# Kernel tuning notes

Measured on AMD Instinct MI355X. Metric: run time of the kernel, lower is better.

The kernel has to match this reference:

```python
import jax, jax.numpy as jnp
import numpy as np

B, S, D, H = 2, 2048, 1024, 16
HD = D // H  # 64


def setup_inputs() -> dict:
    key = jax.random.key(0)
    ks = jax.random.split(key, 12)
    scale = 1.0 / np.sqrt(D)
    inp = {
        "input_query": jax.random.normal(ks[0], (B, S, D), jnp.float32),
        "input_key": jax.random.normal(ks[1], (B, S, D), jnp.float32),
        "input_value": jax.random.normal(ks[2], (B, S, D), jnp.float32),
        "mask": jax.random.randint(ks[3], (B, 1, S), 0, 2, jnp.int32),
        # torch nn.Linear params: y = x @ W.T + b, W shape (out, in)
        "wq": jax.random.uniform(ks[4], (D, D), jnp.float32, -scale, scale),
        "bq": jax.random.uniform(ks[5], (D,), jnp.float32, -scale, scale),
        "wk": jax.random.uniform(ks[6], (D, D), jnp.float32, -scale, scale),
        "bk": jax.random.uniform(ks[7], (D,), jnp.float32, -scale, scale),
        "wv": jax.random.uniform(ks[8], (D, D), jnp.float32, -scale, scale),
        "bv": jax.random.uniform(ks[9], (D,), jnp.float32, -scale, scale),
        "wo": jax.random.uniform(ks[10], (D, D), jnp.float32, -scale, scale),
        "bo": jax.random.uniform(ks[11], (D,), jnp.float32, -scale, scale),
    }
    return inp


def _split_heads(x):
    # (B, S, D) -> (B, H, S, HD)
    return x.reshape(B, S, H, HD).transpose(0, 2, 1, 3)


def reference(input_query, input_key, input_value, mask, wq, bq, wk, bk, wv, bv, wo, bo):
    q = _split_heads(input_query @ wq.T + bq)
    k = _split_heads(input_key @ wk.T + bk)
    v = _split_heads(input_value @ wv.T + bv)

    # scaled dot-product attention (materializes [B,H,S,S] as the original does)
    scores = jnp.einsum("bhqd,bhkd->bhqk", q, k) / np.sqrt(HD).astype(np.float32)
    # mask: (B, 1, S) -> unsqueeze(1) -> (B, 1, 1, S); fill -1e9 where mask == 0
    m = mask[:, None, :, :]
    scores = jnp.where(m == 0, jnp.float32(-1e9), scores)
    p_attn = jax.nn.softmax(scores, axis=-1)  # dropout is identity (rate 0 / eval)

    out = jnp.einsum("bhqk,bhkd->bhqd", p_attn, v)
    out = out.transpose(0, 2, 1, 3).reshape(B, S, D)
    return out @ wo.T + bo
```

## Files before the change

kernel.cpp:

```cpp
#include <hip/hip_runtime.h>
#include <math.h>

#define BB 2
#define SS 2048
#define DD 1024
#define HH 16
#define HD 64

typedef short short8 __attribute__((ext_vector_type(8)));
typedef float floatx4 __attribute__((ext_vector_type(4)));
typedef float floatx16 __attribute__((ext_vector_type(16)));
typedef unsigned int uintx2 __attribute__((ext_vector_type(2)));

__device__ inline ushort f2bf_rne(float x) {
    union { float f; unsigned u; } v; v.f = x;
    unsigned r = v.u + 0x7FFFu + ((v.u >> 16) & 1u);
    return (ushort)(r >> 16);
}
__device__ inline unsigned cvt_pk_bf16(float lo, float hi) {
    unsigned r;
    asm("v_cvt_pk_bf16_f32 %0, %1, %2" : "=v"(r) : "v"(lo), "v"(hi));
    return r;
}
__device__ inline short8 mk_pf(uintx2 x, uintx2 y) {
    union { unsigned u[4]; short8 s; } t;
    t.u[0] = x[0]; t.u[1] = y[0]; t.u[2] = x[1]; t.u[3] = y[1];
    return t.s;
}

#define GLD16(gp, lp) __builtin_amdgcn_global_load_lds( \
    (const __attribute__((address_space(1))) void*)(gp), \
    (__attribute__((address_space(3))) void*)(lp), 16, 0, 0)

__global__ __launch_bounds__(256)
void convert_bf16(const float* __restrict__ xq, const float* __restrict__ xk,
                  const float* __restrict__ xv,
                  const float* __restrict__ wq, const float* __restrict__ wk,
                  const float* __restrict__ wv, const float* __restrict__ wo,
                  ushort* __restrict__ Xq, ushort* __restrict__ Xk,
                  ushort* __restrict__ Xv,
                  ushort* __restrict__ Wq, ushort* __restrict__ Wk,
                  ushort* __restrict__ Wv, ushort* __restrict__ Wo)
{
    const int z = blockIdx.z;
    const size_t i = ((size_t)blockIdx.x * 256 + threadIdx.x) * 8;

    const float* src;
    ushort* dst;
    size_t off;
    if (z < 3) {
        src = (z == 0) ? xq : (z == 1) ? xk : xv;
        dst = (z == 0) ? Xq : (z == 1) ? Xk : Xv;
        off = i;
    } else {
        const int seg = (int)(i >> 20);
        off = i & ((1u << 20) - 1);
        src = (seg == 0) ? wq : (seg == 1) ? wk : (seg == 2) ? wv : wo;
        dst = (seg == 0) ? Wq : (seg == 1) ? Wk : (seg == 2) ? Wv : Wo;
    }
    float x[8];
    *(float4*)&x[0] = *(const float4*)(src + off);
    *(float4*)&x[4] = *(const float4*)(src + off + 4);
    short8 h8;
#pragma unroll
    for (int j = 0; j < 8; ++j) h8[j] = (short)f2bf_rne(x[j]);
    *(short8*)&dst[off] = h8;
}

__global__ __launch_bounds__(256, 3)
void qkv_gemm(const ushort* __restrict__ Xq, const ushort* __restrict__ Xk,
              const ushort* __restrict__ Xv,
              const ushort* __restrict__ Wq, const ushort* __restrict__ Wk,
              const ushort* __restrict__ Wv,
              const float* __restrict__ bq, const float* __restrict__ bk,
              const float* __restrict__ bv, const int* __restrict__ mask,
              ushort* __restrict__ Qo, ushort* __restrict__ Ko,
              ushort* __restrict__ Vo, float qscale)
{
    __shared__ __align__(16) ushort SMEM[8704];
#define ALDS(r, c) SMEM[(r) * 32 + (c)]
#define BLDS(r, c) SMEM[4096 + (r) * 32 + (c)]
#define EPI(r, c)  SMEM[(r) * 136 + (c)]

    const int z   = blockIdx.z;
    const int tid = threadIdx.x;

    const ushort* X    = (z == 0) ? Xq : (z == 1) ? Xk : Xv;
    const ushort* W    = (z == 0) ? Wq : (z == 1) ? Wk : Wv;
    const float*  bias = (z == 0) ? bq : (z == 1) ? bk : bv;
    const float   osc  = (z == 0) ? qscale : 1.0f;

    const int lane = tid & 63;
    const int wave = tid >> 6;
    const int wr = wave >> 1;
    const int wc = wave & 1;
    const int lt = lane & 15;
    const int lq = lane >> 4;
    const int m0 = blockIdx.y * 128;
    const int n0 = blockIdx.x * 128;

    floatx4 acc[4][4];
#pragma unroll
    for (int mi = 0; mi < 4; ++mi)
#pragma unroll
        for (int ni = 0; ni < 4; ++ni) acc[mi][ni] = (floatx4)0.0f;

    const int srow = tid >> 2;
    const int sc   = (tid & 3) << 3;
    const ushort* gA0 = X + (size_t)(m0 + srow) * DD + sc;
    const ushort* gA1 = X + (size_t)(m0 + 64 + srow) * DD + sc;
    const ushort* gB0 = W + (size_t)(n0 + srow) * DD + sc;
    const ushort* gB1 = W + (size_t)(n0 + 64 + srow) * DD + sc;

    for (int k0 = 0; k0 < DD; k0 += 32) {
        __syncthreads();
        GLD16(gA0 + k0, &ALDS(srow, sc));
        GLD16(gA1 + k0, &ALDS(64 + srow, sc));
        GLD16(gB0 + k0, &BLDS(srow, sc));
        GLD16(gB1 + k0, &BLDS(64 + srow, sc));
        __syncthreads();

        short8 af[4], bf_[4];
#pragma unroll
        for (int mi = 0; mi < 4; ++mi)
            af[mi] = *(const short8*)&ALDS(wr * 64 + mi * 16 + lt, lq * 8);
#pragma unroll
        for (int ni = 0; ni < 4; ++ni)
            bf_[ni] = *(const short8*)&BLDS(wc * 64 + ni * 16 + lt, lq * 8);

#pragma unroll
        for (int mi = 0; mi < 4; ++mi)
#pragma unroll
            for (int ni = 0; ni < 4; ++ni)
                acc[mi][ni] = __builtin_amdgcn_mfma_f32_16x16x32_bf16(af[mi], bf_[ni], acc[mi][ni], 0, 0, 0);
    }

    float bbv[4];
#pragma unroll
    for (int ni = 0; ni < 4; ++ni) bbv[ni] = bias[n0 + wc * 64 + ni * 16 + lt];

    if (z == 2) {
#pragma unroll
        for (int half = 0; half < 2; ++half) {
            __syncthreads();
            if (wc == half) {
#pragma unroll
                for (int mi = 0; mi < 4; ++mi) {
                    const int mb  = m0 + wr * 64 + mi * 16 + lq * 4;
                    const int bb_ = mb >> 11;
                    const int s   = mb & (SS - 1);
                    const int4 mm = *(const int4*)(mask + bb_ * SS + s);
                    const float mf[4] = {(float)mm.x, (float)mm.y, (float)mm.z, (float)mm.w};
#pragma unroll
                    for (int ni = 0; ni < 4; ++ni)
#pragma unroll
                        for (int r = 0; r < 4; ++r)
                            EPI(ni * 16 + lt, wr * 64 + mi * 16 + lq * 4 + r) =
                                f2bf_rne((acc[mi][ni][r] + bbv[ni]) * mf[r]);
                }
            }
            __syncthreads();
            const int b_ = m0 >> 11;
            const int sB = m0 & (SS - 1);
#pragma unroll
            for (int u = 0; u < 4; ++u) {
                const int idx = u * 256 + tid;
                const int row = idx >> 4;
                const int sg  = (idx & 15) << 3;
                const short8 v = *(const short8*)&EPI(row, sg);
                const int n = n0 + half * 64 + row;
                const int h = n >> 6;
                *(short8*)&Vo[((size_t)(b_ * HH + h) * HD + (n & 63)) * SS + sB + sg] = v;
            }
        }
    } else {
        ushort* C = z ? Ko : Qo;
#pragma unroll
        for (int half = 0; half < 2; ++half) {
            __syncthreads();
            if (wr == half) {
#pragma unroll
                for (int mi = 0; mi < 4; ++mi) {
                    const int mb  = m0 + half * 64 + mi * 16 + lq * 4;
                    const int bb_ = mb >> 11;
                    const int s   = mb & (SS - 1);
                    float mf[4] = {1.0f, 1.0f, 1.0f, 1.0f};
                    if (z == 1) {
                        const int4 mm = *(const int4*)(mask + bb_ * SS + s);
                        mf[0] = (float)mm.x; mf[1] = (float)mm.y;
                        mf[2] = (float)mm.z; mf[3] = (float)mm.w;
                    }
#pragma unroll
                    for (int ni = 0; ni < 4; ++ni)
#pragma unroll
                        for (int r = 0; r < 4; ++r)
                            EPI(mi * 16 + lq * 4 + r, wc * 64 + ni * 16 + lt) =
                                f2bf_rne((acc[mi][ni][r] + bbv[ni]) * osc * mf[r]);
                }
            }
            __syncthreads();
#pragma unroll
            for (int u = 0; u < 4; ++u) {
                const int idx = u * 256 + tid;
                const int row = idx >> 4;
                const int cg  = (idx & 15) << 3;
                const short8 v = *(const short8*)&EPI(row, cg);
                const int m = m0 + half * 64 + row;
                const int n = n0 + cg;
                const int h = n >> 6;
                const int b_ = m >> 11;
                const int s  = m & (SS - 1);
                *(short8*)&C[((size_t)(b_ * HH + h) * SS + s) * HD + (n & 63)] = v;
            }
        }
    }
#undef ALDS
#undef BLDS
#undef EPI
}

#define LDV 68

__global__ __launch_bounds__(256, 4)
void attn_mfma(const ushort* __restrict__ Qb, const ushort* __restrict__ Kb,
               const ushort* __restrict__ Vt, const int* __restrict__ mask,
               ushort* __restrict__ Ob)
{
    __shared__ __align__(16) ushort KVlds[4][64][LDV];
    __shared__ int Wsum[4];

    const int tid  = threadIdx.x;
    const int lane = tid & 63;
    const int wave = tid >> 6;
    const int ll   = lane & 31;
    const int hi   = lane >> 5;
    const int qh   = wave & 1;
    const int ks   = wave >> 1;

    const int bid    = blockIdx.x;
    const int xcd    = bid & 7;
    const int slot   = bid >> 3;
    const int bhloc  = slot >> 5;
    const int qi     = slot & 31;
    const int bh     = xcd * 4 + bhloc;
    const int b      = bh >> 4;
    const int q0     = qi * 64;

    const size_t sbase = (size_t)bh * SS * HD;
    const size_t vbase = (size_t)bh * HD * SS;

    {
        const int4 ma = *(const int4*)(mask + b * SS + tid * 8);
        const int4 mb = *(const int4*)(mask + b * SS + tid * 8 + 4);
        int s = ma.x + ma.y + ma.z + ma.w + mb.x + mb.y + mb.z + mb.w;
#pragma unroll
        for (int w = 32; w >= 1; w >>= 1) s += __shfl_xor(s, w);
        if (lane == 0) Wsum[wave] = s;
    }

    short8 ones;
#pragma unroll
    for (int j = 0; j < 8; ++j) ones[j] = (short)0x3F80;

    short8 qf[4];
    {
        const size_t qrow = sbase + (size_t)(q0 + qh * 32 + ll) * HD;
#pragma unroll
        for (int dc = 0; dc < 4; ++dc)
            qf[dc] = *(const short8*)(Qb + qrow + dc * 16 + hi * 8);
    }

    floatx16 oacc[2];
    oacc[0] = (floatx16)0.0f;
    oacc[1] = (floatx16)0.0f;
    floatx16 lacc = (floatx16)0.0f;

    const int srow = tid >> 2;
    const int sp16 = (tid & 3) << 4;

    short8 kr0, kr1, vr0, vr1;

    {
        const size_t koff = sbase + (size_t)srow * HD + sp16;
        kr0 = *(const short8*)(Kb + koff);
        kr1 = *(const short8*)(Kb + koff + 8);
        const size_t voff = vbase + (size_t)srow * SS + sp16;
        vr0 = *(const short8*)(Vt + voff);
        vr1 = *(const short8*)(Vt + voff + 8);
        *(short8*)&KVlds[0][srow][sp16]     = kr0;
        *(short8*)&KVlds[0][srow][sp16 + 8] = kr1;
        *(short8*)&KVlds[2][srow][sp16]     = vr0;
        *(short8*)&KVlds[2][srow][sp16 + 8] = vr1;
    }

    const int NT = SS / 64;
    for (int kt = 0; kt < NT; ++kt) {
        const int cur = kt & 1;
        __syncthreads();

        if (kt + 1 < NT) {
            const int k0n = (kt + 1) * 64;
            const size_t koff = sbase + (size_t)(k0n + srow) * HD + sp16;
            kr0 = *(const short8*)(Kb + koff);
            kr1 = *(const short8*)(Kb + koff + 8);
            const size_t voff = vbase + (size_t)srow * SS + k0n + sp16;
            vr0 = *(const short8*)(Vt + voff);
            vr1 = *(const short8*)(Vt + voff + 8);
        }

        short8 kf[4];
#pragma unroll
        for (int dc = 0; dc < 4; ++dc)
            kf[dc] = *(const short8*)&KVlds[cur][ks * 32 + ll][dc * 16 + hi * 8];

        floatx16 sacc = (floatx16)0.0f;
        __builtin_amdgcn_s_setprio(1);
#pragma unroll
        for (int dc = 0; dc < 4; ++dc)
            sacc = __builtin_amdgcn_mfma_f32_32x32x16_bf16(kf[dc], qf[dc], sacc, 0, 0, 0);
        __builtin_amdgcn_s_setprio(0);

        float p[16];
#pragma unroll
        for (int r = 0; r < 16; ++r) p[r] = __builtin_amdgcn_exp2f(sacc[r]);

        const unsigned pk_a = cvt_pk_bf16(p[0],  p[1]);
        const unsigned pk_b = cvt_pk_bf16(p[2],  p[3]);
        const unsigned pk_c = cvt_pk_bf16(p[4],  p[5]);
        const unsigned pk_d = cvt_pk_bf16(p[6],  p[7]);
        const unsigned pk_e = cvt_pk_bf16(p[8],  p[9]);
        const unsigned pk_f = cvt_pk_bf16(p[10], p[11]);
        const unsigned pk_g = cvt_pk_bf16(p[12], p[13]);
        const unsigned pk_h = cvt_pk_bf16(p[14], p[15]);
        const uintx2 s1 = __builtin_amdgcn_permlane32_swap(pk_a, pk_c, false, false);
        const uintx2 s2 = __builtin_amdgcn_permlane32_swap(pk_b, pk_d, false, false);
        const uintx2 s3 = __builtin_amdgcn_permlane32_swap(pk_e, pk_g, false, false);
        const uintx2 s4 = __builtin_amdgcn_permlane32_swap(pk_f, pk_h, false, false);
        const short8 pf0 = mk_pf(s1, s2);
        const short8 pf1 = mk_pf(s3, s4);

        __builtin_amdgcn_s_setprio(1);
        lacc = __builtin_amdgcn_mfma_f32_32x32x16_bf16(pf0, ones, lacc, 0, 0, 0);
        lacc = __builtin_amdgcn_mfma_f32_32x32x16_bf16(pf1, ones, lacc, 0, 0, 0);
#pragma unroll
        for (int dn = 0; dn < 2; ++dn) {
            const short8 vf0 = *(const short8*)&KVlds[2 + cur][dn * 32 + ll][ks * 32 + hi * 8];
            const short8 vf1 = *(const short8*)&KVlds[2 + cur][dn * 32 + ll][ks * 32 + 16 + hi * 8];
            oacc[dn] = __builtin_amdgcn_mfma_f32_32x32x16_bf16(pf0, vf0, oacc[dn], 0, 0, 0);
            oacc[dn] = __builtin_amdgcn_mfma_f32_32x32x16_bf16(pf1, vf1, oacc[dn], 0, 0, 0);
        }
        __builtin_amdgcn_s_setprio(0);

        if (kt + 1 < NT) {
            const int nxt = cur ^ 1;
            *(short8*)&KVlds[nxt][srow][sp16]     = kr0;
            *(short8*)&KVlds[nxt][srow][sp16 + 8] = kr1;
            *(short8*)&KVlds[2 + nxt][srow][sp16]     = vr0;
            *(short8*)&KVlds[2 + nxt][srow][sp16 + 8] = vr1;
        }
    }

    float* Cmb = (float*)&KVlds[0][0][0];
    __syncthreads();
    if (ks == 1) {
#pragma unroll
        for (int dn = 0; dn < 2; ++dn)
#pragma unroll
            for (int r = 0; r < 16; ++r)
                Cmb[((qh * 2 + dn) * 16 + r) * 64 + lane] = oacc[dn][r];
#pragma unroll
        for (int r = 0; r < 16; ++r)
            Cmb[4096 + (qh * 16 + r) * 64 + lane] = lacc[r];
    }
    __syncthreads();
    if (ks == 0) {
#pragma unroll
        for (int dn = 0; dn < 2; ++dn)
#pragma unroll
            for (int r = 0; r < 16; ++r)
                oacc[dn][r] += Cmb[((qh * 2 + dn) * 16 + r) * 64 + lane];
#pragma unroll
        for (int r = 0; r < 16; ++r)
            lacc[r] += Cmb[4096 + (qh * 16 + r) * 64 + lane];

        const int h = bh & 15;
        const float nmf = (float)(SS - (Wsum[0] + Wsum[1] + Wsum[2] + Wsum[3]));
        float linv[16];
#pragma unroll
        for (int r = 0; r < 16; ++r) linv[r] = 1.0f / (lacc[r] - nmf);
#pragma unroll
        for (int dn = 0; dn < 2; ++dn)
#pragma unroll
            for (int r = 0; r < 16; ++r) {
                const int q = q0 + qh * 32 + (r & 3) + 8 * (r >> 2) + 4 * hi;
                Ob[(size_t)(b * SS + q) * DD + h * HD + dn * 32 + ll] =
                    f2bf_rne(oacc[dn][r] * linv[r]);
            }
    }
}

__global__ __launch_bounds__(256, 3)
void o_gemm(const ushort* __restrict__ A, const ushort* __restrict__ B,
            const float* __restrict__ bias, float* __restrict__ out)
{
    __shared__ __align__(16) ushort sA[128][32];
    __shared__ __align__(16) ushort sB[64][32];

    const int tid  = threadIdx.x;
    const int lane = tid & 63;
    const int wave = tid >> 6;
    const int wr = wave >> 1;
    const int wc = wave & 1;
    const int lt = lane & 15;
    const int lq = lane >> 4;
    const int m0 = blockIdx.y * 128;
    const int n0 = blockIdx.x * 64;

    floatx4 acc[4][2];
#pragma unroll
    for (int mi = 0; mi < 4; ++mi)
#pragma unroll
        for (int ni = 0; ni < 2; ++ni) acc[mi][ni] = (floatx4)0.0f;

    const int srow = tid >> 2;
    const int sc   = (tid & 3) << 3;
    const ushort* gA0 = A + (size_t)(m0 + srow) * DD + sc;
    const ushort* gA1 = A + (size_t)(m0 + 64 + srow) * DD + sc;
    const ushort* gB0 = B + (size_t)(n0 + srow) * DD + sc;

    for (int k0 = 0; k0 < DD; k0 += 32) {
        __syncthreads();
        GLD16(gA0 + k0, &sA[srow][sc]);
        GLD16(gA1 + k0, &sA[64 + srow][sc]);
        GLD16(gB0 + k0, &sB[srow][sc]);
        __syncthreads();

        short8 af[4], bf_[2];
#pragma unroll
        for (int mi = 0; mi < 4; ++mi)
            af[mi] = *(const short8*)&sA[wr * 64 + mi * 16 + lt][lq * 8];
#pragma unroll
        for (int ni = 0; ni < 2; ++ni)
            bf_[ni] = *(const short8*)&sB[wc * 32 + ni * 16 + lt][lq * 8];

#pragma unroll
        for (int mi = 0; mi < 4; ++mi)
#pragma unroll
            for (int ni = 0; ni < 2; ++ni)
                acc[mi][ni] = __builtin_amdgcn_mfma_f32_16x16x32_bf16(af[mi], bf_[ni], acc[mi][ni], 0, 0, 0);
    }

#pragma unroll
    for (int mi = 0; mi < 4; ++mi)
#pragma unroll
        for (int ni = 0; ni < 2; ++ni) {
            const int n = n0 + wc * 32 + ni * 16 + lt;
            const float bb = bias[n];
#pragma unroll
            for (int r = 0; r < 4; ++r) {
                const int m = m0 + wr * 64 + mi * 16 + lq * 4 + r;
                out[(size_t)m * DD + n] = acc[mi][ni][r] + bb;
            }
        }
}

extern "C" void kernel_launch(void* const* d_in, const int* in_sizes, int n_in,
                              void* d_out, int out_size, void* d_ws, size_t ws_size,
                              hipStream_t stream) {
    const float* xq   = (const float*)d_in[0];
    const float* xk   = (const float*)d_in[1];
    const float* xv   = (const float*)d_in[2];
    const int*   mask = (const int*)d_in[3];
    const float* wq   = (const float*)d_in[4];
    const float* bq   = (const float*)d_in[5];
    const float* wk   = (const float*)d_in[6];
    const float* bk   = (const float*)d_in[7];
    const float* wv   = (const float*)d_in[8];
    const float* bv   = (const float*)d_in[9];
    const float* wo   = (const float*)d_in[10];
    const float* bo   = (const float*)d_in[11];
    float* out = (float*)d_out;

    const size_t n = (size_t)BB * SS * DD;
    const size_t w1 = (size_t)DD * DD;

    ushort* Xqb = (ushort*)d_ws;
    ushort* Xkb = Xqb + n;
    ushort* Xvb = Xkb + n;
    ushort* Kb  = Xvb + n;
    ushort* Vt  = Kb + n;
    ushort* Wob = Vt + n;
    ushort* Ob  = Xqb;

    ushort* Qb  = (ushort*)out;
    ushort* Wqb = Qb + n;
    ushort* Wkb = Wqb + w1;
    ushort* Wvb = Wkb + w1;

    const float qscale = 0.125f * 1.44269504088896340736f;

    dim3 gc(2048, 1, 4);
    convert_bf16<<<gc, 256, 0, stream>>>(xq, xk, xv, wq, wk, wv, wo,
                                         Xqb, Xkb, Xvb, Wqb, Wkb, Wvb, Wob);

    dim3 g1(DD / 128, (BB * SS) / 128, 3);
    qkv_gemm<<<g1, 256, 0, stream>>>(Xqb, Xkb, Xvb, Wqb, Wkb, Wvb,
                                     bq, bk, bv, mask, Qb, Kb, Vt, qscale);

    attn_mfma<<<dim3(1024), 256, 0, stream>>>(Qb, Kb, Vt, mask, Ob);

    dim3 g2(DD / 64, (BB * SS) / 128);
    o_gemm<<<g2, 256, 0, stream>>>(Ob, Wob, bo, out);
}
```

Measured before the change: 219.4 us.

## Remap GEMM blocks across XCDs and drop LDS-staged epilogue stores

Both projection GEMMs move to a 1D grid whose block index is remapped so consecutive blocks on each of the 8 XCDs cover neighbouring tiles, meant to improve L2 reuse of A/B tiles. The QKV epilogue no longer stages results through shared memory with extra barriers. It writes directly from accumulators to global memory: 8-byte packed stores for V-transpose and scalar 2-byte scattered stores for Q/K. This removes LDS traffic and syncs but makes the Q/K global writes much less coalesced.

New measurement: 217.6 us. About the same (-0.8%).

```diff
diff --git a/kernel.cpp b/kernel.cpp
--- a/kernel.cpp
+++ b/kernel.cpp
@@ -77,13 +77,16 @@
               ushort* __restrict__ Qo, ushort* __restrict__ Ko,
               ushort* __restrict__ Vo, float qscale)
 {
-    __shared__ __align__(16) ushort SMEM[8704];
-#define ALDS(r, c) SMEM[(r) * 32 + (c)]
-#define BLDS(r, c) SMEM[4096 + (r) * 32 + (c)]
-#define EPI(r, c)  SMEM[(r) * 136 + (c)]
-
-    const int z   = blockIdx.z;
+    __shared__ __align__(16) ushort Alds[128][32];
+    __shared__ __align__(16) ushort Blds[128][32];
+
     const int tid = threadIdx.x;
+
+    const int wg  = (blockIdx.x & 7) * 96 + (blockIdx.x >> 3);
+    const int z   = wg >> 8;
+    const int rem = wg & 255;
+    const int m0  = (rem >> 3) * 128;
+    const int n0  = (rem & 7) * 128;
 
     const ushort* X    = (z == 0) ? Xq : (z == 1) ? Xk : Xv;
     const ushort* W    = (z == 0) ? Wq : (z == 1) ? Wk : Wv;
@@ -96,8 +99,6 @@
     const int wc = wave & 1;
     const int lt = lane & 15;
     const int lq = lane >> 4;
-    const int m0 = blockIdx.y * 128;
-    const int n0 = blockIdx.x * 128;
 
     floatx4 acc[4][4];
 #pragma unroll
@@ -114,19 +115,19 @@
 
     for (int k0 = 0; k0 < DD; k0 += 32) {
         __syncthreads();
-        GLD16(gA0 + k0, &ALDS(srow, sc));
-        GLD16(gA1 + k0, &ALDS(64 + srow, sc));
-        GLD16(gB0 + k0, &BLDS(srow, sc));
-        GLD16(gB1 + k0, &BLDS(64 + srow, sc));
+        GLD16(gA0 + k0, &Alds[srow][sc]);
+        GLD16(gA1 + k0, &Alds[64 + srow][sc]);
+        GLD16(gB0 + k0, &Blds[srow][sc]);
+        GLD16(gB1 + k0, &Blds[64 + srow][sc]);
         __syncthreads();
 
         short8 af[4], bf_[4];
 #pragma unroll
         for (int mi = 0; mi < 4; ++mi)
-            af[mi] = *(const short8*)&ALDS(wr * 64 + mi * 16 + lt, lq * 8);
+            af[mi] = *(const short8*)&Alds[wr * 64 + mi * 16 + lt][lq * 8];
 #pragma unroll
         for (int ni = 0; ni < 4; ++ni)
-            bf_[ni] = *(const short8*)&BLDS(wc * 64 + ni * 16 + lt, lq * 8);
+            bf_[ni] = *(const short8*)&Blds[wc * 64 + ni * 16 + lt][lq * 8];
 
 #pragma unroll
         for (int mi = 0; mi < 4; ++mi)
@@ -141,82 +142,50 @@
 
     if (z == 2) {
 #pragma unroll
-        for (int half = 0; half < 2; ++half) {
-            __syncthreads();
-            if (wc == half) {
-#pragma unroll
-                for (int mi = 0; mi < 4; ++mi) {
-                    const int mb  = m0 + wr * 64 + mi * 16 + lq * 4;
-                    const int bb_ = mb >> 11;
-                    const int s   = mb & (SS - 1);
-                    const int4 mm = *(const int4*)(mask + bb_ * SS + s);
-                    const float mf[4] = {(float)mm.x, (float)mm.y, (float)mm.z, (float)mm.w};
-#pragma unroll
-                    for (int ni = 0; ni < 4; ++ni)
-#pragma unroll
-                        for (int r = 0; r < 4; ++r)
-                            EPI(ni * 16 + lt, wr * 64 + mi * 16 + lq * 4 + r) =
-                                f2bf_rne((acc[mi][ni][r] + bbv[ni]) * mf[r]);
+        for (int mi = 0; mi < 4; ++mi) {
+            const int mb  = m0 + wr * 64 + mi * 16 + lq * 4;
+            const int bb_ = mb >> 11;
+            const int s   = mb & (SS - 1);
+            const int4 mm = *(const int4*)(mask + bb_ * SS + s);
+            const float mf0 = (float)mm.x, mf1 = (float)mm.y;
+            const float mf2 = (float)mm.z, mf3 = (float)mm.w;
+#pragma unroll
+            for (int ni = 0; ni < 4; ++ni) {
+                const int n = n0 + wc * 64 + ni * 16 + lt;
+                const int h = n >> 6;
+                ushort4 pack;
+                pack.x = f2bf_rne((acc[mi][ni][0] + bbv[ni]) * mf0);
+                pack.y = f2bf_rne((acc[mi][ni][1] + bbv[ni]) * mf1);
+                pack.z = f2bf_rne((acc[mi][ni][2] + bbv[ni]) * mf2);
+                pack.w = f2bf_rne((acc[mi][ni][3] + bbv[ni]) * mf3);
+                *(ushort4*)&Vo[(size_t)((bb_ * HH + h) * HD + (n & 63)) * SS + s] = pack;
+            }
+        }
+    } else {
+        ushort* C = z ? Ko : Qo;
+#pragma unroll
+        for (int mi = 0; mi < 4; ++mi) {
+            const int mb  = m0 + wr * 64 + mi * 16 + lq * 4;
+            const int bb_ = mb >> 11;
+            const int s   = mb & (SS - 1);
+            float mf[4] = {1.0f, 1.0f, 1.0f, 1.0f};
+            if (z == 1) {
+                const int4 mm = *(const int4*)(mask + bb_ * SS + s);
+                mf[0] = (float)mm.x; mf[1] = (float)mm.y;
+                mf[2] = (float)mm.z; mf[3] = (float)mm.w;
+            }
+#pragma unroll
+            for (int ni = 0; ni < 4; ++ni) {
+                const int n = n0 + wc * 64 + ni * 16 + lt;
+                const int h = n >> 6;
+#pragma unroll
+                for (int r = 0; r < 4; ++r) {
+                    C[(size_t)((bb_ * HH + h) * SS + (s + r)) * HD + (n & 63)] =
+                        f2bf_rne((acc[mi][ni][r] + bbv[ni]) * osc * mf[r]);
                 }
             }
-            __syncthreads();
-            const int b_ = m0 >> 11;
-            const int sB = m0 & (SS - 1);
-#pragma unroll
-            for (int u = 0; u < 4; ++u) {
-                const int idx = u * 256 + tid;
-                const int row = idx >> 4;
-                const int sg  = (idx & 15) << 3;
-                const short8 v = *(const short8*)&EPI(row, sg);
-                const int n = n0 + half * 64 + row;
-                const int h = n >> 6;
-                *(short8*)&Vo[((size_t)(b_ * HH + h) * HD + (n & 63)) * SS + sB + sg] = v;
-            }
-        }
-    } else {
-        ushort* C = z ? Ko : Qo;
-#pragma unroll
-        for (int half = 0; half < 2; ++half) {
-            __syncthreads();
-            if (wr == half) {
-#pragma unroll
-                for (int mi = 0; mi < 4; ++mi) {
-                    const int mb  = m0 + half * 64 + mi * 16 + lq * 4;
-                    const int bb_ = mb >> 11;
-                    const int s   = mb & (SS - 1);
-                    float mf[4] = {1.0f, 1.0f, 1.0f, 1.0f};
-                    if (z == 1) {
-                        const int4 mm = *(const int4*)(mask + bb_ * SS + s);
-                        mf[0] = (float)mm.x; mf[1] = (float)mm.y;
-                        mf[2] = (float)mm.z; mf[3] = (float)mm.w;
-                    }
-#pragma unroll
-                    for (int ni = 0; ni < 4; ++ni)
-#pragma unroll
-                        for (int r = 0; r < 4; ++r)
-                            EPI(mi * 16 + lq * 4 + r, wc * 64 + ni * 16 + lt) =
-                                f2bf_rne((acc[mi][ni][r] + bbv[ni]) * osc * mf[r]);
-                }
-            }
-            __syncthreads();
-#pragma unroll
-            for (int u = 0; u < 4; ++u) {
-                const int idx = u * 256 + tid;
-                const int row = idx >> 4;
-                const int cg  = (idx & 15) << 3;
-                const short8 v = *(const short8*)&EPI(row, cg);
-                const int m = m0 + half * 64 + row;
-                const int n = n0 + cg;
-                const int h = n >> 6;
-                const int b_ = m >> 11;
-                const int s  = m & (SS - 1);
-                *(short8*)&C[((size_t)(b_ * HH + h) * SS + s) * HD + (n & 63)] = v;
-            }
-        }
-    }
-#undef ALDS
-#undef BLDS
-#undef EPI
+        }
+    }
 }
 
 #define LDV 68
@@ -413,8 +382,10 @@
     const int wc = wave & 1;
     const int lt = lane & 15;
     const int lq = lane >> 4;
-    const int m0 = blockIdx.y * 128;
-    const int n0 = blockIdx.x * 64;
+
+    const int wg = (blockIdx.x & 7) * 64 + (blockIdx.x >> 3);
+    const int m0 = (wg >> 4) * 128;
+    const int n0 = (wg & 15) * 64;
 
     floatx4 acc[4][2];
 #pragma unroll
@@ -503,12 +474,10 @@
     convert_bf16<<<gc, 256, 0, stream>>>(xq, xk, xv, wq, wk, wv, wo,
                                          Xqb, Xkb, Xvb, Wqb, Wkb, Wvb, Wob);
 
-    dim3 g1(DD / 128, (BB * SS) / 128, 3);
-    qkv_gemm<<<g1, 256, 0, stream>>>(Xqb, Xkb, Xvb, Wqb, Wkb, Wvb,
-                                     bq, bk, bv, mask, Qb, Kb, Vt, qscale);
+    qkv_gemm<<<dim3(768), 256, 0, stream>>>(Xqb, Xkb, Xvb, Wqb, Wkb, Wvb,
+                                            bq, bk, bv, mask, Qb, Kb, Vt, qscale);
 
     attn_mfma<<<dim3(1024), 256, 0, stream>>>(Qb, Kb, Vt, mask, Ob);
 
-    dim3 g2(DD / 64, (BB * SS) / 128);
-    o_gemm<<<g2, 256, 0, stream>>>(Ob, Wob, bo, out);
-}
+    o_gemm<<<dim3(512), 256, 0, stream>>>(Ob, Wob, bo, out);
+}
```
